# Kernel optimization log

Hardware: AMD Instinct MI355X
Metric: run time of the kernel (lower is better)

Reference implementation:

```python
import jax, jax.numpy as jnp
import numpy as np

D_IN = 768
D_MODEL = 768
NUM_HEADS = 12
DEPTH = D_MODEL // NUM_HEADS


def setup_inputs() -> dict:
    key = jax.random.key(0)
    ks = jax.random.split(key, 9)
    B, N = 2, 2048
    s_in = 1.0 / np.sqrt(D_IN)
    s_md = 1.0 / np.sqrt(D_MODEL)
    return {
        "x": jax.random.normal(ks[0], (B, N, D_IN), dtype=jnp.float32),
        "wq": jax.random.normal(ks[1], (D_IN, D_MODEL), dtype=jnp.float32) * s_in,
        "bq": jax.random.normal(ks[2], (D_MODEL,), dtype=jnp.float32) * 0.02,
        "wk": jax.random.normal(ks[3], (D_IN, D_MODEL), dtype=jnp.float32) * s_in,
        "bk": jax.random.normal(ks[4], (D_MODEL,), dtype=jnp.float32) * 0.02,
        "wv": jax.random.normal(ks[5], (D_IN, D_MODEL), dtype=jnp.float32) * s_in,
        "bv": jax.random.normal(ks[6], (D_MODEL,), dtype=jnp.float32) * 0.02,
        "wo": jax.random.normal(ks[7], (D_MODEL, D_MODEL), dtype=jnp.float32) * s_md,
        "bo": jax.random.normal(ks[8], (D_MODEL,), dtype=jnp.float32) * 0.02,
    }


def reference(x, wq, bq, wk, bk, wv, bv, wo, bo):
    B, N, _ = x.shape
    H, D = NUM_HEADS, DEPTH
    # project and split heads: [B,N,H,D] -> [B,H,N,D]
    q = (x @ wq + bq).reshape(B, N, H, D).transpose(0, 2, 1, 3)
    k = (x @ wk + bk).reshape(B, N, H, D).transpose(0, 2, 1, 3)
    v = (x @ wv + bv).reshape(B, N, H, D).transpose(0, 2, 1, 3)
    scale = 1.0 / jnp.sqrt(jnp.asarray(D, dtype=q.dtype))
    attn = jnp.einsum('bhnd,bhmd->bhnm', q, k) * scale  # [B,H,N,N]
    attn = jax.nn.softmax(attn, axis=-1)
    z = jnp.einsum('bhnm,bhmd->bhnd', attn, v)
    z = z.transpose(0, 2, 1, 3).reshape(B, N, H * D)
    return z @ wo + bo
```

## Files before the change

### kernel.cpp

```cpp
#include <hip/hip_runtime.h>
#include <hip/hip_bf16.h>
#include <math.h>

#define NH 12
#define DH 64
#define BB 2
#define NN 2048
#define DM 768

typedef short v8s __attribute__((ext_vector_type(8)));
typedef float v4f __attribute__((ext_vector_type(4)));

__device__ __forceinline__ unsigned short f2bf(float f) {
    union { float f; unsigned u; } x; x.f = f;
    unsigned r = x.u + 0x7fffu + ((x.u >> 16) & 1u);
    return (unsigned short)(r >> 16);
}

__device__ __forceinline__ int cvtpk(float lo, float hi2) {
    int r;
    asm("v_cvt_pk_bf16_f32 %0, %1, %2" : "=v"(r) : "v"(lo), "v"(hi2));
    return r;
}

__device__ __forceinline__ void glds16(const void* g, void* l) {
    __builtin_amdgcn_global_load_lds((const __attribute__((address_space(1))) void*)g,
                                     (__attribute__((address_space(3))) void*)l, 16, 0, 0);
}

__global__ __launch_bounds__(256) void cast_fused_k(
    const float* __restrict__ x, unsigned short* __restrict__ xb,
    const float* __restrict__ w0, const float* __restrict__ w1,
    const float* __restrict__ w2, const float* __restrict__ w3,
    unsigned short* __restrict__ o0, unsigned short* __restrict__ o1,
    unsigned short* __restrict__ o2, unsigned short* __restrict__ o3) {
    __shared__ unsigned short t[64][65];
    int bid = blockIdx.x;
    if (bid < 3072) {
        int i = (bid * 256 + threadIdx.x) * 4;
        float4 v = *(const float4*)(x + i);
        ushort4 o;
        o.x = f2bf(v.x); o.y = f2bf(v.y); o.z = f2bf(v.z); o.w = f2bf(v.w);
        *(ushort4*)(xb + i) = o;
        return;
    }
    int idx = bid - 3072;
    int m = idx / 144, xt = idx % 144;
    const float* in; unsigned short* out;
    switch (m) {
        case 0: in = w0; out = o0; break;
        case 1: in = w1; out = o1; break;
        case 2: in = w2; out = o2; break;
        default: in = w3; out = o3; break;
    }
    int kt = xt / 12, ct = xt % 12;
    int rr = threadIdx.x >> 4, cc = threadIdx.x & 15;
#pragma unroll
    for (int it = 0; it < 4; it++) {
        int row = kt * 64 + it * 16 + rr;
        int col = ct * 64 + cc * 4;
        float4 v = *(const float4*)(in + row * 768 + col);
        t[it * 16 + rr][cc * 4 + 0] = f2bf(v.x);
        t[it * 16 + rr][cc * 4 + 1] = f2bf(v.y);
        t[it * 16 + rr][cc * 4 + 2] = f2bf(v.z);
        t[it * 16 + rr][cc * 4 + 3] = f2bf(v.w);
    }
    __syncthreads();
#pragma unroll
    for (int it = 0; it < 4; it++) {
        int c_l = it * 16 + rr;
        int k_l = cc * 4;
        ushort4 o;
        o.x = t[k_l + 0][c_l];
        o.y = t[k_l + 1][c_l];
        o.z = t[k_l + 2][c_l];
        o.w = t[k_l + 3][c_l];
        *(ushort4*)(out + (ct * 64 + c_l) * 768 + kt * 64 + k_l) = o;
    }
}

__global__ __launch_bounds__(512) void qkv_gemm_k(
    const unsigned short* __restrict__ xb,
    const unsigned short* __restrict__ wqT, const unsigned short* __restrict__ wkT,
    const unsigned short* __restrict__ wvT,
    const float* __restrict__ bq, const float* __restrict__ bk, const float* __restrict__ bv,
    unsigned short* __restrict__ q, unsigned short* __restrict__ k, unsigned short* __restrict__ vT) {
    __shared__ unsigned short Abuf[3][128 * 32];
    __shared__ unsigned short Bbuf[3][128 * 32];

    int lin = blockIdx.x;
    int swz = (lin & 7) * 72 + (lin >> 3);
    int ctile = swz % 18;
    int mtile = swz / 18;
    int mat = ctile / 6;
    int col0 = (ctile % 6) * 128;
    const unsigned short* Bsrc = (mat == 0) ? wqT : ((mat == 1) ? wkT : wvT);
    const float* bias = (mat == 0) ? bq : ((mat == 1) ? bk : bv);

    int tid = threadIdx.x;
    int w = tid >> 6, l = tid & 63;
    int q16 = l & 15, g = l >> 4;
    int wr = w >> 2, wc = w & 3;

    int srow = tid >> 2;
    int ss = tid & 3;
    int c16s = ss ^ ((srow >> 1) & 3);

    auto stage = [&](int tt, int buf) {
        int k0 = tt * 32;
        glds16(xb + (mtile * 128 + srow) * 768 + k0 + (c16s << 3),
               (char*)&Abuf[buf][0] + tid * 16);
        glds16(Bsrc + (col0 + srow) * 768 + k0 + (c16s << 3),
               (char*)&Bbuf[buf][0] + tid * 16);
    };

    v4f zero = {0.f, 0.f, 0.f, 0.f};
    v4f acc[4][2];
#pragma unroll
    for (int i = 0; i < 4; i++)
#pragma unroll
        for (int j = 0; j < 2; j++) acc[i][j] = zero;

    stage(0, 0);
    stage(1, 1);
    asm volatile("s_waitcnt vmcnt(2)" ::: "memory");
    __builtin_amdgcn_s_barrier();
    asm volatile("" ::: "memory");

    int rd = 0;
    for (int tt = 0; tt < 24; ++tt) {
        int st = rd + 2; if (st >= 3) st -= 3;
        if (tt + 2 < 24) stage(tt + 2, st);
        const char* Ab = (const char*)&Abuf[rd][0];
        const char* Bb = (const char*)&Bbuf[rd][0];
        v8s af[4], bf[2];
#pragma unroll
        for (int f = 0; f < 4; f++) {
            int arow = wr * 64 + f * 16 + q16;
            af[f] = *(const v8s*)(Ab + arow * 64 + ((g ^ ((arow >> 1) & 3)) << 4));
        }
#pragma unroll
        for (int j = 0; j < 2; j++) {
            int brow = wc * 32 + j * 16 + q16;
            bf[j] = *(const v8s*)(Bb + brow * 64 + ((g ^ ((brow >> 1) & 3)) << 4));
        }
        __builtin_amdgcn_s_setprio(1);
#pragma unroll
        for (int i = 0; i < 4; i++)
#pragma unroll
            for (int j = 0; j < 2; j++)
                acc[i][j] = __builtin_amdgcn_mfma_f32_16x16x32_bf16(af[i], bf[j], acc[i][j], 0, 0, 0);
        __builtin_amdgcn_s_setprio(0);
        asm volatile("s_waitcnt vmcnt(2)" ::: "memory");
        __builtin_amdgcn_s_barrier();
        asm volatile("" ::: "memory");
        rd = (rd + 1 == 3) ? 0 : rd + 1;
    }

    const float QSCL = 0.125f * 1.44269504088896340736f;
#pragma unroll
    for (int i = 0; i < 4; i++)
#pragma unroll
        for (int j = 0; j < 2; j++)
#pragma unroll
            for (int r = 0; r < 4; r++) {
                int gr = mtile * 128 + wr * 64 + i * 16 + 4 * g + r;
                int gcl = col0 + wc * 32 + j * 16 + q16;
                int b = gr / NN, n = gr % NN;
                int h = gcl / DH, d = gcl % DH;
                int bh = b * NH + h;
                float v = acc[i][j][r] + bias[gcl];
                if (mat == 0)      q[(bh * NN + n) * DH + d]  = f2bf(v * QSCL);
                else if (mat == 1) k[(bh * NN + n) * DH + d]  = f2bf(v);
                else               vT[(bh * DH + d) * NN + n] = f2bf(v);
            }
}

__global__ __launch_bounds__(512) void attn_k(
    const unsigned short* __restrict__ q, const unsigned short* __restrict__ k,
    const unsigned short* __restrict__ vT, unsigned short* __restrict__ z) {
    __shared__ __align__(16) char Kb[2][2][4096];
    __shared__ __align__(16) char Vb[2][2][4096];
    __shared__ unsigned short plds[8][16][36];

    int bh = blockIdx.x % 24;
    int qt = blockIdx.x / 24;
    int b = bh / NH, h = bh % NH;
    int tid = threadIdx.x;
    int w = tid >> 6, l = tid & 63;
    int q16 = l & 15, g = l >> 4;
    int ws = w & 3, hf = w >> 2;

    const unsigned short* qp = q + (size_t)bh * NN * DH;
    const unsigned short* kp = k + (size_t)bh * NN * DH;
    const unsigned short* vp = vT + (size_t)bh * DH * NN;
    int qrow = qt * 64 + ws * 16 + q16;

    v8s qf0 = *(const v8s*)(qp + qrow * DH + 8 * g);
    v8s qf1 = *(const v8s*)(qp + qrow * DH + 32 + 8 * g);

    v8s ones;
#pragma unroll
    for (int i = 0; i < 8; i++) ones[i] = (short)0x3F80;

    int hf_s = tid >> 8;
    int s8 = tid & 255;
    int row_s = s8 >> 3, sl = s8 & 7;
    int kc16 = (sl ^ (row_s & 7)) & 7;
    int vj = sl ^ (row_s & 7);
    int vd = row_s + ((vj >> 2) << 5);
    int vkw = vj & 3;

    auto stage = [&](int t, int buf) {
        int kv0 = hf_s * (NN / 2) + t * 32;
        glds16(kp + (kv0 + row_s) * DH + (kc16 << 3), &Kb[hf_s][buf][s8 * 16]);
        glds16(vp + (size_t)vd * NN + kv0 + vkw * 8, &Vb[hf_s][buf][s8 * 16]);
    };

    v4f zero = {0.f, 0.f, 0.f, 0.f};
    float mrow = -INFINITY;
    v4f o[4];
    v4f osum = zero;
#pragma unroll
    for (int dt = 0; dt < 4; dt++) o[dt] = zero;

    stage(0, 0);
    __syncthreads();

    for (int t = 0; t < 32; ++t) {
        int cur = t & 1;
        if (t + 1 < 32) stage(t + 1, cur ^ 1);

        const char* kb = &Kb[hf][cur][0];
        const char* vb = &Vb[hf][cur][0];

        v4f st[2];
#pragma unroll
        for (int ct = 0; ct < 2; ct++) {
            int krow = ct * 16 + q16;
            v8s kf0 = *(const v8s*)(kb + krow * 128 + ((g ^ (krow & 7)) << 4));
            v8s kf1 = *(const v8s*)(kb + krow * 128 + (((4 + g) ^ (krow & 7)) << 4));
            __builtin_amdgcn_s_setprio(1);
            st[ct] = __builtin_amdgcn_mfma_f32_16x16x32_bf16(kf0, qf0, zero, 0, 0, 0);
            st[ct] = __builtin_amdgcn_mfma_f32_16x16x32_bf16(kf1, qf1, st[ct], 0, 0, 0);
            __builtin_amdgcn_s_setprio(0);
        }

        float ma = fmaxf(fmaxf(st[0][0], st[0][1]), st[0][2]);
        float mb = fmaxf(fmaxf(st[0][3], st[1][0]), st[1][1]);
        float vmax = fmaxf(fmaxf(ma, mb), fmaxf(st[1][2], st[1][3]));
        vmax = fmaxf(vmax, __shfl_xor(vmax, 16));
        vmax = fmaxf(vmax, __shfl_xor(vmax, 32));

        if (!__all(vmax <= mrow + 8.f)) {
            float mn = fmaxf(mrow, vmax);
            float sc = exp2f(mrow - mn);
#pragma unroll
            for (int dt = 0; dt < 4; dt++)
#pragma unroll
                for (int r = 0; r < 4; r++) o[dt][r] *= sc;
            osum[0] *= sc;
            mrow = mn;
        }

#pragma unroll
        for (int ct = 0; ct < 2; ct++) {
            float p0 = exp2f(st[ct][0] - mrow);
            float p1 = exp2f(st[ct][1] - mrow);
            float p2 = exp2f(st[ct][2] - mrow);
            float p3 = exp2f(st[ct][3] - mrow);
            union { int i[2]; short4 s; } u;
            u.i[0] = cvtpk(p0, p1);
            u.i[1] = cvtpk(p2, p3);
            *(short4*)(&plds[w][q16][ct * 16 + 4 * g]) = u.s;
        }

        v8s pf0 = *(const v8s*)(&plds[w][q16][8 * g]);

        osum = __builtin_amdgcn_mfma_f32_16x16x32_bf16(ones, pf0, osum, 0, 0, 0);

        __builtin_amdgcn_s_setprio(1);
#pragma unroll
        for (int dt = 0; dt < 4; dt++) {
            int dcol = dt * 16 + q16;
            int rr = dcol & 31;
            int sl2 = (((dcol >> 5) << 2) + g) ^ (rr & 7);
            v8s vf = *(const v8s*)(vb + rr * 128 + (sl2 << 4));
            o[dt] = __builtin_amdgcn_mfma_f32_16x16x32_bf16(vf, pf0, o[dt], 0, 0, 0);
        }
        __builtin_amdgcn_s_setprio(0);
        __syncthreads();
    }

    float* po = (float*)&Kb[0][0][0];
    float* pm = (float*)&Vb[0][0][0];
    float* pl = pm + 64;
    int row = ws * 16 + q16;

    if (hf == 1) {
#pragma unroll
        for (int dt = 0; dt < 4; dt++)
#pragma unroll
            for (int r = 0; r < 4; r++)
                po[row * 64 + dt * 16 + 4 * g + r] = o[dt][r];
        if (g == 0) { pm[row] = mrow; pl[row] = osum[0]; }
    }
    __syncthreads();
    if (hf == 0) {
        float m1 = pm[row], l1 = pl[row];
        float ms = fmaxf(mrow, m1);
        float a0 = exp2f(mrow - ms), a1 = exp2f(m1 - ms);
        float inv = 1.f / (osum[0] * a0 + l1 * a1);
        int n = qt * 64 + ws * 16 + q16;
#pragma unroll
        for (int dt = 0; dt < 4; dt++) {
            short4 s4;
            s4.x = (short)f2bf((o[dt][0] * a0 + po[row * 64 + dt * 16 + 4 * g + 0] * a1) * inv);
            s4.y = (short)f2bf((o[dt][1] * a0 + po[row * 64 + dt * 16 + 4 * g + 1] * a1) * inv);
            s4.z = (short)f2bf((o[dt][2] * a0 + po[row * 64 + dt * 16 + 4 * g + 2] * a1) * inv);
            s4.w = (short)f2bf((o[dt][3] * a0 + po[row * 64 + dt * 16 + 4 * g + 3] * a1) * inv);
            *(short4*)(&z[((size_t)(b * NN + n)) * DM + h * DH + dt * 16 + 4 * g]) = s4;
        }
    }
}

__global__ __launch_bounds__(256) void out_gemm_k(
    const unsigned short* __restrict__ zb, const unsigned short* __restrict__ woT,
    const float* __restrict__ bo, float* __restrict__ out) {
    __shared__ unsigned short Abuf[3][64 * 32];
    __shared__ unsigned short Bbuf[3][64 * 32];

    int lin = blockIdx.x;
    int swz = (lin & 7) * 96 + (lin >> 3);
    int mtile = swz / 12;
    int ctile = swz % 12;
    int col0 = ctile * 64;

    int tid = threadIdx.x;
    int w = tid >> 6, l = tid & 63;
    int q16 = l & 15, g = l >> 4;
    int wr = w >> 1, wc = w & 1;

    int srow = tid >> 2;
    int ss = tid & 3;
    int c16s = ss ^ ((srow >> 1) & 3);

    auto stage = [&](int tt, int buf) {
        int k0 = tt * 32;
        glds16(zb + (mtile * 64 + srow) * 768 + k0 + (c16s << 3),
               (char*)&Abuf[buf][0] + tid * 16);
        glds16(woT + (col0 + srow) * 768 + k0 + (c16s << 3),
               (char*)&Bbuf[buf][0] + tid * 16);
    };

    v4f zero = {0.f, 0.f, 0.f, 0.f};
    v4f acc[2][2];
#pragma unroll
    for (int i = 0; i < 2; i++)
#pragma unroll
        for (int j = 0; j < 2; j++) acc[i][j] = zero;

    stage(0, 0);
    stage(1, 1);
    asm volatile("s_waitcnt vmcnt(2)" ::: "memory");
    __builtin_amdgcn_s_barrier();
    asm volatile("" ::: "memory");

    int rd = 0;
    for (int tt = 0; tt < 24; ++tt) {
        int st = rd + 2; if (st >= 3) st -= 3;
        if (tt + 2 < 24) stage(tt + 2, st);
        const char* Ab = (const char*)&Abuf[rd][0];
        const char* Bb = (const char*)&Bbuf[rd][0];
        v8s af[2], bf[2];
#pragma unroll
        for (int f = 0; f < 2; f++) {
            int arow = wr * 32 + f * 16 + q16;
            af[f] = *(const v8s*)(Ab + arow * 64 + ((g ^ ((arow >> 1) & 3)) << 4));
            int brow = wc * 32 + f * 16 + q16;
            bf[f] = *(const v8s*)(Bb + brow * 64 + ((g ^ ((brow >> 1) & 3)) << 4));
        }
        __builtin_amdgcn_s_setprio(1);
#pragma unroll
        for (int i = 0; i < 2; i++)
#pragma unroll
            for (int j = 0; j < 2; j++)
                acc[i][j] = __builtin_amdgcn_mfma_f32_16x16x32_bf16(af[i], bf[j], acc[i][j], 0, 0, 0);
        __builtin_amdgcn_s_setprio(0);
        asm volatile("s_waitcnt vmcnt(2)" ::: "memory");
        __builtin_amdgcn_s_barrier();
        asm volatile("" ::: "memory");
        rd = (rd + 1 == 3) ? 0 : rd + 1;
    }

#pragma unroll
    for (int i = 0; i < 2; i++)
#pragma unroll
        for (int j = 0; j < 2; j++)
#pragma unroll
            for (int r = 0; r < 4; r++) {
                int gr = mtile * 64 + wr * 32 + i * 16 + 4 * g + r;
                int gc = col0 + wc * 32 + j * 16 + q16;
                out[gr * 768 + gc] = acc[i][j][r] + bo[gc];
            }
}

extern "C" void kernel_launch(void* const* d_in, const int* in_sizes, int n_in,
                              void* d_out, int out_size, void* d_ws, size_t ws_size,
                              hipStream_t stream) {
    const float* x  = (const float*)d_in[0];
    const float* wq = (const float*)d_in[1];
    const float* bq = (const float*)d_in[2];
    const float* wk = (const float*)d_in[3];
    const float* bk = (const float*)d_in[4];
    const float* wv = (const float*)d_in[5];
    const float* bv = (const float*)d_in[6];
    const float* wo = (const float*)d_in[7];
    const float* bo = (const float*)d_in[8];
    float* out = (float*)d_out;

    const int NX = BB * NN * DM;
    const int NW = 768 * 768;

    unsigned short* wsp = (unsigned short*)d_ws;
    unsigned short* xb  = wsp;
    unsigned short* wqT = xb + NX;
    unsigned short* wkT = wqT + NW;
    unsigned short* wvT = wkT + NW;
    unsigned short* woT = wvT + NW;
    unsigned short* qb  = woT + NW;
    unsigned short* kb  = qb + NX;
    unsigned short* vTb = kb + NX;
    unsigned short* zb  = vTb + NX;

    cast_fused_k<<<3648, 256, 0, stream>>>(x, xb, wq, wk, wv, wo, wqT, wkT, wvT, woT);
    qkv_gemm_k<<<576, 512, 0, stream>>>(xb, wqT, wkT, wvT, bq, bk, bv, qb, kb, vTb);
    attn_k<<<BB * NH * (NN / 64), 512, 0, stream>>>(qb, kb, vTb, zb);
    out_gemm_k<<<768, 256, 0, stream>>>(zb, woT, bo, out);
}
```

Before: 117.0 us.

## Process two query sub-tiles per wave in attention, halving block threads

The attention kernel now uses 256 threads per block instead of 512. Each wave handles 32 query rows (two 16-row sub-tiles) rather than 16, so every K and V fragment read from shared memory feeds twice as many MFMAs. Staging loops over both KV halves per thread, and the final merge folds the normalization into two coefficients. This cuts LDS traffic per MFMA and the number of waves that synchronize on barriers. In exchange it raises register pressure, since accumulators and scores double, and there are fewer waves available to hide latency.

```diff
diff --git a/kernel.cpp b/kernel.cpp
--- a/kernel.cpp
+++ b/kernel.cpp
@@ -176,12 +176,12 @@
             }
 }
 
-__global__ __launch_bounds__(512) void attn_k(
+__global__ __launch_bounds__(256) void attn_k(
     const unsigned short* __restrict__ q, const unsigned short* __restrict__ k,
     const unsigned short* __restrict__ vT, unsigned short* __restrict__ z) {
     __shared__ __align__(16) char Kb[2][2][4096];
     __shared__ __align__(16) char Vb[2][2][4096];
-    __shared__ unsigned short plds[8][16][36];
+    __shared__ unsigned short plds[4][32][36];
 
     int bh = blockIdx.x % 24;
     int qt = blockIdx.x / 24;
@@ -189,40 +189,48 @@
     int tid = threadIdx.x;
     int w = tid >> 6, l = tid & 63;
     int q16 = l & 15, g = l >> 4;
-    int ws = w & 3, hf = w >> 2;
+    int ws = w & 1, hf = w >> 1;
 
     const unsigned short* qp = q + (size_t)bh * NN * DH;
     const unsigned short* kp = k + (size_t)bh * NN * DH;
     const unsigned short* vp = vT + (size_t)bh * DH * NN;
-    int qrow = qt * 64 + ws * 16 + q16;
-
-    v8s qf0 = *(const v8s*)(qp + qrow * DH + 8 * g);
-    v8s qf1 = *(const v8s*)(qp + qrow * DH + 32 + 8 * g);
+    int qrow = qt * 64 + ws * 32 + q16;
+
+    v8s qf[2][2];
+#pragma unroll
+    for (int qi = 0; qi < 2; qi++) {
+        qf[qi][0] = *(const v8s*)(qp + (qrow + 16 * qi) * DH + 8 * g);
+        qf[qi][1] = *(const v8s*)(qp + (qrow + 16 * qi) * DH + 32 + 8 * g);
+    }
 
     v8s ones;
 #pragma unroll
     for (int i = 0; i < 8; i++) ones[i] = (short)0x3F80;
 
-    int hf_s = tid >> 8;
-    int s8 = tid & 255;
+    int s8 = tid;
     int row_s = s8 >> 3, sl = s8 & 7;
-    int kc16 = (sl ^ (row_s & 7)) & 7;
+    int kc16 = sl ^ (row_s & 7);
     int vj = sl ^ (row_s & 7);
     int vd = row_s + ((vj >> 2) << 5);
     int vkw = vj & 3;
 
     auto stage = [&](int t, int buf) {
-        int kv0 = hf_s * (NN / 2) + t * 32;
-        glds16(kp + (kv0 + row_s) * DH + (kc16 << 3), &Kb[hf_s][buf][s8 * 16]);
-        glds16(vp + (size_t)vd * NN + kv0 + vkw * 8, &Vb[hf_s][buf][s8 * 16]);
+#pragma unroll
+        for (int hs = 0; hs < 2; ++hs) {
+            int kv0 = hs * (NN / 2) + t * 32;
+            glds16(kp + (kv0 + row_s) * DH + (kc16 << 3), &Kb[hs][buf][s8 * 16]);
+            glds16(vp + (size_t)vd * NN + kv0 + vkw * 8, &Vb[hs][buf][s8 * 16]);
+        }
     };
 
     v4f zero = {0.f, 0.f, 0.f, 0.f};
-    float mrow = -INFINITY;
-    v4f o[4];
-    v4f osum = zero;
-#pragma unroll
-    for (int dt = 0; dt < 4; dt++) o[dt] = zero;
+    float mrow[2] = {-INFINITY, -INFINITY};
+    v4f o[4][2];
+    v4f osum[2] = {zero, zero};
+#pragma unroll
+    for (int dt = 0; dt < 4; dt++)
+#pragma unroll
+        for (int qi = 0; qi < 2; qi++) o[dt][qi] = zero;
 
     stage(0, 0);
     __syncthreads();
@@ -234,50 +242,66 @@
         const char* kb = &Kb[hf][cur][0];
         const char* vb = &Vb[hf][cur][0];
 
-        v4f st[2];
+        v4f st[2][2];
 #pragma unroll
         for (int ct = 0; ct < 2; ct++) {
             int krow = ct * 16 + q16;
             v8s kf0 = *(const v8s*)(kb + krow * 128 + ((g ^ (krow & 7)) << 4));
             v8s kf1 = *(const v8s*)(kb + krow * 128 + (((4 + g) ^ (krow & 7)) << 4));
             __builtin_amdgcn_s_setprio(1);
-            st[ct] = __builtin_amdgcn_mfma_f32_16x16x32_bf16(kf0, qf0, zero, 0, 0, 0);
-            st[ct] = __builtin_amdgcn_mfma_f32_16x16x32_bf16(kf1, qf1, st[ct], 0, 0, 0);
+#pragma unroll
+            for (int qi = 0; qi < 2; qi++) {
+                st[ct][qi] = __builtin_amdgcn_mfma_f32_16x16x32_bf16(kf0, qf[qi][0], zero, 0, 0, 0);
+                st[ct][qi] = __builtin_amdgcn_mfma_f32_16x16x32_bf16(kf1, qf[qi][1], st[ct][qi], 0, 0, 0);
+            }
             __builtin_amdgcn_s_setprio(0);
         }
 
-        float ma = fmaxf(fmaxf(st[0][0], st[0][1]), st[0][2]);
-        float mb = fmaxf(fmaxf(st[0][3], st[1][0]), st[1][1]);
-        float vmax = fmaxf(fmaxf(ma, mb), fmaxf(st[1][2], st[1][3]));
-        vmax = fmaxf(vmax, __shfl_xor(vmax, 16));
-        vmax = fmaxf(vmax, __shfl_xor(vmax, 32));
-
-        if (!__all(vmax <= mrow + 8.f)) {
-            float mn = fmaxf(mrow, vmax);
-            float sc = exp2f(mrow - mn);
-#pragma unroll
-            for (int dt = 0; dt < 4; dt++)
-#pragma unroll
-                for (int r = 0; r < 4; r++) o[dt][r] *= sc;
-            osum[0] *= sc;
-            mrow = mn;
-        }
-
-#pragma unroll
-        for (int ct = 0; ct < 2; ct++) {
-            float p0 = exp2f(st[ct][0] - mrow);
-            float p1 = exp2f(st[ct][1] - mrow);
-            float p2 = exp2f(st[ct][2] - mrow);
-            float p3 = exp2f(st[ct][3] - mrow);
-            union { int i[2]; short4 s; } u;
-            u.i[0] = cvtpk(p0, p1);
-            u.i[1] = cvtpk(p2, p3);
-            *(short4*)(&plds[w][q16][ct * 16 + 4 * g]) = u.s;
-        }
-
-        v8s pf0 = *(const v8s*)(&plds[w][q16][8 * g]);
-
-        osum = __builtin_amdgcn_mfma_f32_16x16x32_bf16(ones, pf0, osum, 0, 0, 0);
+        float vmax[2];
+#pragma unroll
+        for (int qi = 0; qi < 2; qi++) {
+            float ma = fmaxf(fmaxf(st[0][qi][0], st[0][qi][1]), st[0][qi][2]);
+            float mb = fmaxf(fmaxf(st[0][qi][3], st[1][qi][0]), st[1][qi][1]);
+            float vm = fmaxf(fmaxf(ma, mb), fmaxf(st[1][qi][2], st[1][qi][3]));
+            vm = fmaxf(vm, __shfl_xor(vm, 16));
+            vm = fmaxf(vm, __shfl_xor(vm, 32));
+            vmax[qi] = vm;
+        }
+
+        if (!__all(vmax[0] <= mrow[0] + 8.f && vmax[1] <= mrow[1] + 8.f)) {
+#pragma unroll
+            for (int qi = 0; qi < 2; qi++) {
+                float mn = fmaxf(mrow[qi], vmax[qi]);
+                float sc = exp2f(mrow[qi] - mn);
+#pragma unroll
+                for (int dt = 0; dt < 4; dt++)
+#pragma unroll
+                    for (int r = 0; r < 4; r++) o[dt][qi][r] *= sc;
+                osum[qi][0] *= sc;
+                mrow[qi] = mn;
+            }
+        }
+
+#pragma unroll
+        for (int qi = 0; qi < 2; qi++)
+#pragma unroll
+            for (int ct = 0; ct < 2; ct++) {
+                float p0 = exp2f(st[ct][qi][0] - mrow[qi]);
+                float p1 = exp2f(st[ct][qi][1] - mrow[qi]);
+                float p2 = exp2f(st[ct][qi][2] - mrow[qi]);
+                float p3 = exp2f(st[ct][qi][3] - mrow[qi]);
+                union { int i[2]; short4 s; } u;
+                u.i[0] = cvtpk(p0, p1);
+                u.i[1] = cvtpk(p2, p3);
+                *(short4*)(&plds[w][qi * 16 + q16][ct * 16 + 4 * g]) = u.s;
+            }
+
+        v8s pf[2];
+        pf[0] = *(const v8s*)(&plds[w][q16][8 * g]);
+        pf[1] = *(const v8s*)(&plds[w][16 + q16][8 * g]);
+
+        osum[0] = __builtin_amdgcn_mfma_f32_16x16x32_bf16(ones, pf[0], osum[0], 0, 0, 0);
+        osum[1] = __builtin_amdgcn_mfma_f32_16x16x32_bf16(ones, pf[1], osum[1], 0, 0, 0);
 
         __builtin_amdgcn_s_setprio(1);
 #pragma unroll
@@ -286,7 +310,9 @@
             int rr = dcol & 31;
             int sl2 = (((dcol >> 5) << 2) + g) ^ (rr & 7);
             v8s vf = *(const v8s*)(vb + rr * 128 + (sl2 << 4));
-            o[dt] = __builtin_amdgcn_mfma_f32_16x16x32_bf16(vf, pf0, o[dt], 0, 0, 0);
+#pragma unroll
+            for (int qi = 0; qi < 2; qi++)
+                o[dt][qi] = __builtin_amdgcn_mfma_f32_16x16x32_bf16(vf, pf[qi], o[dt][qi], 0, 0, 0);
         }
         __builtin_amdgcn_s_setprio(0);
         __syncthreads();
@@ -295,31 +321,39 @@
     float* po = (float*)&Kb[0][0][0];
     float* pm = (float*)&Vb[0][0][0];
     float* pl = pm + 64;
-    int row = ws * 16 + q16;
 
     if (hf == 1) {
 #pragma unroll
-        for (int dt = 0; dt < 4; dt++)
-#pragma unroll
-            for (int r = 0; r < 4; r++)
-                po[row * 64 + dt * 16 + 4 * g + r] = o[dt][r];
-        if (g == 0) { pm[row] = mrow; pl[row] = osum[0]; }
+        for (int qi = 0; qi < 2; qi++) {
+            int row = ws * 32 + qi * 16 + q16;
+#pragma unroll
+            for (int dt = 0; dt < 4; dt++)
+#pragma unroll
+                for (int r = 0; r < 4; r++)
+                    po[row * 64 + dt * 16 + 4 * g + r] = o[dt][qi][r];
+            if (g == 0) { pm[row] = mrow[qi]; pl[row] = osum[qi][0]; }
+        }
     }
     __syncthreads();
     if (hf == 0) {
-        float m1 = pm[row], l1 = pl[row];
-        float ms = fmaxf(mrow, m1);
-        float a0 = exp2f(mrow - ms), a1 = exp2f(m1 - ms);
-        float inv = 1.f / (osum[0] * a0 + l1 * a1);
-        int n = qt * 64 + ws * 16 + q16;
-#pragma unroll
-        for (int dt = 0; dt < 4; dt++) {
-            short4 s4;
-            s4.x = (short)f2bf((o[dt][0] * a0 + po[row * 64 + dt * 16 + 4 * g + 0] * a1) * inv);
-            s4.y = (short)f2bf((o[dt][1] * a0 + po[row * 64 + dt * 16 + 4 * g + 1] * a1) * inv);
-            s4.z = (short)f2bf((o[dt][2] * a0 + po[row * 64 + dt * 16 + 4 * g + 2] * a1) * inv);
-            s4.w = (short)f2bf((o[dt][3] * a0 + po[row * 64 + dt * 16 + 4 * g + 3] * a1) * inv);
-            *(short4*)(&z[((size_t)(b * NN + n)) * DM + h * DH + dt * 16 + 4 * g]) = s4;
+#pragma unroll
+        for (int qi = 0; qi < 2; qi++) {
+            int row = ws * 32 + qi * 16 + q16;
+            float m1 = pm[row], l1 = pl[row];
+            float ms = fmaxf(mrow[qi], m1);
+            float a0 = exp2f(mrow[qi] - ms), a1 = exp2f(m1 - ms);
+            float inv = 1.f / (osum[qi][0] * a0 + l1 * a1);
+            float ca = a0 * inv, cb = a1 * inv;
+            int n = qt * 64 + row;
+#pragma unroll
+            for (int dt = 0; dt < 4; dt++) {
+                short4 s4;
+                s4.x = (short)f2bf(o[dt][qi][0] * ca + po[row * 64 + dt * 16 + 4 * g + 0] * cb);
+                s4.y = (short)f2bf(o[dt][qi][1] * ca + po[row * 64 + dt * 16 + 4 * g + 1] * cb);
+                s4.z = (short)f2bf(o[dt][qi][2] * ca + po[row * 64 + dt * 16 + 4 * g + 2] * cb);
+                s4.w = (short)f2bf(o[dt][qi][3] * ca + po[row * 64 + dt * 16 + 4 * g + 3] * cb);
+                *(short4*)(&z[((size_t)(b * NN + n)) * DM + h * DH + dt * 16 + 4 * g]) = s4;
+            }
         }
     }
 }
@@ -435,6 +469,6 @@
 
     cast_fused_k<<<3648, 256, 0, stream>>>(x, xb, wq, wk, wv, wo, wqT, wkT, wvT, woT);
     qkv_gemm_k<<<576, 512, 0, stream>>>(xb, wqT, wkT, wvT, bq, bk, bv, qb, kb, vTb);
-    attn_k<<<BB * NH * (NN / 64), 512, 0, stream>>>(qb, kb, vTb, zb);
+    attn_k<<<BB * NH * (NN / 64), 256, 0, stream>>>(qb, kb, vTb, zb);
     out_gemm_k<<<768, 256, 0, stream>>>(zb, woT, bo, out);
 }
```

Result: no change. 118.9 us (+1.6%).
